# Kernel tuning notes

Measured on AMD Instinct MI355X. Metric: run time of the kernel, lower is better.

## Reference

```python
import jax, jax.numpy as jnp
import numpy as np

N_NODES = 100000
D_FEAT = 64
HIDDEN = 64
N_CLASSES = 16
N_EDGES = 1600000


def setup_inputs() -> dict:
    key = jax.random.key(0)
    ks = jax.random.split(key, 8)
    x = jax.random.normal(ks[0], (N_NODES, D_FEAT), dtype=jnp.float32)
    edge_index = jax.random.randint(ks[1], (2, N_EDGES), 0, N_NODES, dtype=jnp.int64)
    s1 = 1.0 / np.sqrt(D_FEAT)
    s2 = 1.0 / np.sqrt(HIDDEN)
    W1 = jax.random.uniform(ks[2], (D_FEAT, HIDDEN), jnp.float32, -s1, s1)
    b1 = jnp.zeros((HIDDEN,), jnp.float32)
    W2 = jax.random.uniform(ks[3], (HIDDEN, HIDDEN), jnp.float32, -s2, s2)
    b2 = jnp.zeros((HIDDEN,), jnp.float32)
    Wfc = jax.random.uniform(ks[4], (HIDDEN, N_CLASSES), jnp.float32, -s2, s2)
    bfc = jax.random.uniform(ks[5], (N_CLASSES,), jnp.float32, -s2, s2)
    return {"x": x, "edge_index": edge_index, "W1": W1, "b1": b1,
            "W2": W2, "b2": b2, "Wfc": Wfc, "bfc": bfc}


def reference(x, edge_index, W1, b1, W2, b2, Wfc, bfc):
    N = x.shape[0]
    loops = jnp.arange(N, dtype=edge_index.dtype)
    # GCNConv adds self-loops by default
    src = jnp.concatenate([edge_index[0], loops])  # message source j
    dst = jnp.concatenate([edge_index[1], loops])  # aggregation target i
    # symmetric normalization: D^{-1/2} (A + I) D^{-1/2}, degree counted on targets
    deg = jax.ops.segment_sum(jnp.ones_like(dst, dtype=x.dtype), dst, num_segments=N)
    dinv = jnp.where(deg > 0, jax.lax.rsqrt(deg), 0.0)
    norm = dinv[src] * dinv[dst]  # [E+N]

    def gcn_conv(h, W, b):
        h = h @ W                              # [N, out] dense transform first (PyG order)
        msg = h[src] * norm[:, None]            # gather + edge scaling, [E+N, out]
        return jax.ops.segment_sum(msg, dst, num_segments=N) + b

    h = jax.nn.relu(gcn_conv(x, W1, b1))
    # dropout is identity in eval mode
    h = jax.nn.relu(gcn_conv(h, W2, b2))
    return jax.nn.softmax(h @ Wfc + bfc, axis=1)
```

## Files before the change

### kernel.cpp

```cpp
#include <hip/hip_runtime.h>
#include <hip/hip_fp16.h>
#include <math.h>

#define NNODES 100000
#define BSHIFT 7
#define BSIZE 128
#define NBUCK ((NNODES + BSIZE - 1) >> BSHIFT)
#define SCAT_BLOCKS 512
#define CHUNKCAP 3328
#define CAPSHIFT 12
#define BCAP (1 << CAPSHIFT)

__global__ __launch_bounds__(1024) void k_init(int* __restrict__ bcur) {
    int k = blockIdx.x * 1024 + threadIdx.x;
    if (k < NBUCK) bcur[k] = k << CAPSHIFT;
}

__global__ __launch_bounds__(256) void k_scatter_fused(const int* __restrict__ src, const int* __restrict__ dst,
                                                       int* __restrict__ bcur, int* __restrict__ staging,
                                                       int E, int chunk) {
    __shared__ int epack[CHUNKCAP];
    __shared__ unsigned short ebuck[CHUNKCAP];
    __shared__ int hist[NBUCK];
    __shared__ int lcur[NBUCK];
    int t = threadIdx.x;
    for (int k = t; k < NBUCK; k += 256) hist[k] = 0;
    __syncthreads();
    int c0 = blockIdx.x * chunk;
    int c1 = min(E, c0 + chunk);
    int n = c1 - c0;
    for (int j = t; j < n; j += 256) {
        int d = dst[c0 + j];
        int s = src[c0 + j];
        int b = d >> BSHIFT;
        epack[j] = (s << BSHIFT) | (d & (BSIZE - 1));
        ebuck[j] = (unsigned short)b;
        atomicAdd(&hist[b], 1);
    }
    __syncthreads();
    for (int k = t; k < NBUCK; k += 256) {
        int c = hist[k];
        lcur[k] = c ? atomicAdd(&bcur[k], c) : 0;
    }
    __syncthreads();
    for (int j = t; j < n; j += 256) {
        int pos = atomicAdd(&lcur[ebuck[j]], 1);
        staging[pos] = epack[j];
    }
}

__global__ __launch_bounds__(256) void k_bucket_csr(const int* __restrict__ staging, const int* __restrict__ bcur,
                                                    int* __restrict__ rowptr, int* __restrict__ rowend,
                                                    int* __restrict__ ssort, float* __restrict__ dinv, int N) {
    __shared__ int lcnt[BSIZE], lpre[BSIZE];
    int b = blockIdx.x, t = threadIdx.x;
    int node0 = b << BSHIFT;
    int bbase = b << CAPSHIFT;
    int bend = bcur[b];
    if (t < BSIZE) lcnt[t] = 0;
    __syncthreads();
    for (int e = bbase + t; e < bend; e += 256)
        atomicAdd(&lcnt[staging[e] & (BSIZE - 1)], 1);
    __syncthreads();
    if (t < BSIZE) lpre[t] = lcnt[t];
    __syncthreads();
    #pragma unroll
    for (int off = 1; off < BSIZE; off <<= 1) {
        int u = 0;
        if (t < BSIZE && t >= off) u = lpre[t - off];
        __syncthreads();
        if (t < BSIZE) lpre[t] += u;
        __syncthreads();
    }
    if (t < BSIZE) {
        int node = node0 + t;
        if (node < N) {
            int beg = bbase + lpre[t] - lcnt[t];
            rowptr[node] = beg;
            rowend[node] = beg + lcnt[t];
            dinv[node] = rsqrtf((float)(lcnt[t] + 1));
        }
        lpre[t] -= lcnt[t];
    }
    __syncthreads();
    for (int e = bbase + t; e < bend; e += 256) {
        int p = staging[e];
        int pos = atomicAdd(&lpre[p & (BSIZE - 1)], 1);
        ssort[bbase + pos] = p >> BSHIFT;
    }
}

__global__ __launch_bounds__(128) void k_transform2(const float* __restrict__ X, const float* __restrict__ W,
                                                    const float* __restrict__ dinv, __half* __restrict__ Gh, int N) {
    __shared__ float Xs[128 * 65];
    __shared__ float Ws[64 * 64];
    int t = threadIdx.x;
    int node0 = blockIdx.x << 7;
    {
        const float4* W4 = (const float4*)W;
        float4* Ws4 = (float4*)Ws;
        #pragma unroll
        for (int j = 0; j < 8; j++) Ws4[j * 128 + t] = W4[j * 128 + t];
    }
    {
        const float4* X4 = (const float4*)X;
        int lim4 = N << 4;
        #pragma unroll
        for (int ii = 0; ii < 16; ii++) {
            int f = ii * 128 + t;
            int row = f >> 4, cq = f & 15;
            int gi = (node0 << 4) + f;
            float4 v = make_float4(0.f, 0.f, 0.f, 0.f);
            if (gi < lim4) v = X4[gi];
            *(float4*)&Xs[row * 65 + cq * 4] = v;
        }
    }
    __syncthreads();
    float acc[64];
    #pragma unroll
    for (int c = 0; c < 64; c++) acc[c] = 0.f;
    int xbase = t * 65;
    for (int k = 0; k < 64; k++) {
        float xk = Xs[xbase + k];
        const float4* wr = (const float4*)&Ws[k * 64];
        #pragma unroll
        for (int cb = 0; cb < 16; cb++) {
            float4 w4 = wr[cb];
            acc[cb * 4 + 0] = fmaf(xk, w4.x, acc[cb * 4 + 0]);
            acc[cb * 4 + 1] = fmaf(xk, w4.y, acc[cb * 4 + 1]);
            acc[cb * 4 + 2] = fmaf(xk, w4.z, acc[cb * 4 + 2]);
            acc[cb * 4 + 3] = fmaf(xk, w4.w, acc[cb * 4 + 3]);
        }
    }
    int node = node0 + t;
    if (node < N) {
        float di = dinv[node];
        float4* g4 = (float4*)(Gh + (size_t)node * 64);
        #pragma unroll
        for (int cb = 0; cb < 8; cb++) {
            float4 pack;
            __half2* hp = (__half2*)&pack;
            #pragma unroll
            for (int q = 0; q < 4; q++)
                hp[q] = __floats2half2_rn(acc[cb * 8 + 2 * q] * di, acc[cb * 8 + 2 * q + 1] * di);
            g4[cb] = pack;
        }
    }
}

__global__ __launch_bounds__(256) void k_agg(const __half* __restrict__ G, const int* __restrict__ rowptr,
                                             const int* __restrict__ rowend, const int* __restrict__ ssort,
                                             const float* __restrict__ dinv, const float* __restrict__ bias,
                                             float* __restrict__ O, int N) {
    int lane = threadIdx.x & 63;
    int wid = threadIdx.x >> 6;
    int sub = lane >> 3;
    int l = lane & 7;
    int i = blockIdx.x * 4 + wid;
    if (i >= N) return;
    int beg = rowptr[i], end = rowend[i];
    float a[8] = {0.f, 0.f, 0.f, 0.f, 0.f, 0.f, 0.f, 0.f};
    int e = beg + sub;
    for (; e + 8 < end; e += 16) {
        int s0 = ssort[e];
        int s1 = ssort[e + 8];
        float4 g0 = *(const float4*)(G + (size_t)s0 * 64 + 8 * l);
        float4 g1 = *(const float4*)(G + (size_t)s1 * 64 + 8 * l);
        const __half2* h0 = (const __half2*)&g0;
        const __half2* h1 = (const __half2*)&g1;
        #pragma unroll
        for (int q = 0; q < 4; q++) {
            float2 f0 = __half22float2(h0[q]);
            float2 f1 = __half22float2(h1[q]);
            a[2 * q]     += f0.x + f1.x;
            a[2 * q + 1] += f0.y + f1.y;
        }
    }
    if (e < end) {
        int s0 = ssort[e];
        float4 g0 = *(const float4*)(G + (size_t)s0 * 64 + 8 * l);
        const __half2* h0 = (const __half2*)&g0;
        #pragma unroll
        for (int q = 0; q < 4; q++) {
            float2 f0 = __half22float2(h0[q]);
            a[2 * q]     += f0.x;
            a[2 * q + 1] += f0.y;
        }
    }
    #pragma unroll
    for (int mask = 8; mask <= 32; mask <<= 1) {
        #pragma unroll
        for (int q = 0; q < 8; q++) a[q] += __shfl_xor(a[q], mask);
    }
    if (sub == 0) {
        float4 gs = *(const float4*)(G + (size_t)i * 64 + 8 * l);
        const __half2* hs = (const __half2*)&gs;
        #pragma unroll
        for (int q = 0; q < 4; q++) {
            float2 fs = __half22float2(hs[q]);
            a[2 * q]     += fs.x;
            a[2 * q + 1] += fs.y;
        }
        float di = dinv[i];
        float4 b0 = *(const float4*)(bias + 8 * l);
        float4 b1 = *(const float4*)(bias + 8 * l + 4);
        float4 o0, o1;
        o0.x = fmaxf(fmaf(di, a[0], b0.x), 0.f);
        o0.y = fmaxf(fmaf(di, a[1], b0.y), 0.f);
        o0.z = fmaxf(fmaf(di, a[2], b0.z), 0.f);
        o0.w = fmaxf(fmaf(di, a[3], b0.w), 0.f);
        o1.x = fmaxf(fmaf(di, a[4], b1.x), 0.f);
        o1.y = fmaxf(fmaf(di, a[5], b1.y), 0.f);
        o1.z = fmaxf(fmaf(di, a[6], b1.z), 0.f);
        o1.w = fmaxf(fmaf(di, a[7], b1.w), 0.f);
        *(float4*)(O + (size_t)i * 64 + 8 * l) = o0;
        *(float4*)(O + (size_t)i * 64 + 8 * l + 4) = o1;
    }
}

__global__ __launch_bounds__(256) void k_fc_softmax(const float* __restrict__ H, const float* __restrict__ Wfc,
                                                    const float* __restrict__ bfc, float* __restrict__ O, int N) {
    __shared__ float wf[64 * 16];
    __shared__ float bf[16];
    int t = threadIdx.x;
    for (int k = t; k < 1024; k += 256) wf[k] = Wfc[k];
    if (t < 16) bf[t] = bfc[t];
    __syncthreads();
    int gid = blockIdx.x * 256 + t;
    int node = gid >> 4;
    int c = gid & 15;
    if (node >= N) return;
    const float4* hv = (const float4*)(H + (size_t)node * 64);
    float acc = bf[c];
    #pragma unroll
    for (int kk = 0; kk < 16; kk++) {
        float4 h4 = hv[kk];
        acc = fmaf(h4.x, wf[(4 * kk + 0) * 16 + c], acc);
        acc = fmaf(h4.y, wf[(4 * kk + 1) * 16 + c], acc);
        acc = fmaf(h4.z, wf[(4 * kk + 2) * 16 + c], acc);
        acc = fmaf(h4.w, wf[(4 * kk + 3) * 16 + c], acc);
    }
    float m = acc;
    #pragma unroll
    for (int mask = 1; mask < 16; mask <<= 1) m = fmaxf(m, __shfl_xor(m, mask));
    float ex = expf(acc - m);
    float s = ex;
    #pragma unroll
    for (int mask = 1; mask < 16; mask <<= 1) s += __shfl_xor(s, mask);
    O[(size_t)node * 16 + c] = ex / s;
}

extern "C" void kernel_launch(void* const* d_in, const int* in_sizes, int n_in,
                              void* d_out, int out_size, void* d_ws, size_t ws_size,
                              hipStream_t stream) {
    const float* x   = (const float*)d_in[0];
    const int*   ei  = (const int*)d_in[1];
    const float* W1  = (const float*)d_in[2];
    const float* b1  = (const float*)d_in[3];
    const float* W2  = (const float*)d_in[4];
    const float* b2  = (const float*)d_in[5];
    const float* Wfc = (const float*)d_in[6];
    const float* bfc = (const float*)d_in[7];
    float* out = (float*)d_out;
    const int N = NNODES;
    const int E = in_sizes[1] / 2;

    char* ws = (char*)d_ws;
    size_t off = 0;
    auto take = [&](size_t bytes) {
        char* p = ws + off;
        off = (off + bytes + 255) & ~(size_t)255;
        return p;
    };
    int*    staging = (int*)take((size_t)NBUCK * BCAP * 4);
    int*    ssort   = (int*)take((size_t)NBUCK * BCAP * 4);
    float*  bufB    = (float*)take((size_t)N * 64 * 4);
    __half* Gh      = (__half*)take((size_t)N * 64 * 2);
    int*    rowptr  = (int*)take((size_t)N * 4);
    int*    rowend  = (int*)take((size_t)N * 4);
    float*  dinv    = (float*)take((size_t)N * 4);
    int*    bcur    = (int*)take((size_t)NBUCK * 4);

    const int* e_src = ei;
    const int* e_dst = ei + E;

    int chunk = (E + SCAT_BLOCKS - 1) / SCAT_BLOCKS;
    k_init<<<1, 1024, 0, stream>>>(bcur);
    k_scatter_fused<<<SCAT_BLOCKS, 256, 0, stream>>>(e_src, e_dst, bcur, staging, E, chunk);
    k_bucket_csr<<<NBUCK, 256, 0, stream>>>(staging, bcur, rowptr, rowend, ssort, dinv, N);

    int tb = (N + 127) / 128;
    k_transform2<<<tb, 128, 0, stream>>>(x, W1, dinv, Gh, N);
    k_agg<<<(N + 3) / 4, 256, 0, stream>>>(Gh, rowptr, rowend, ssort, dinv, b1, bufB, N);
    k_transform2<<<tb, 128, 0, stream>>>(bufB, W2, dinv, Gh, N);
    k_agg<<<(N + 3) / 4, 256, 0, stream>>>(Gh, rowptr, rowend, ssort, dinv, b2, bufB, N);
    k_fc_softmax<<<(N * 16 + 255) / 256, 256, 0, stream>>>(bufB, Wfc, bfc, out, N);
}
```

Baseline: 224.5 us.

## Restructure dense transform: per-lane output column with weights in registers

The node-feature transform kernel is rewritten so each lane owns one output column and keeps its 64-entry weight column in registers, while a wavefront walks 32 nodes four at a time, reading X rows from LDS as broadcasts. This replaces the old scheme of one node per thread with 64 accumulators and the W tile held in LDS. Blocks grow to 256 threads, and dinv is staged in shared memory. Output is now written as one half per lane, coalesced across the wavefront, instead of 16-byte packed rows per thread. This may cost store efficiency.

```diff
diff --git a/kernel.cpp b/kernel.cpp
--- a/kernel.cpp
+++ b/kernel.cpp
@@ -90,60 +90,67 @@
     }
 }
 
-__global__ __launch_bounds__(128) void k_transform2(const float* __restrict__ X, const float* __restrict__ W,
+__global__ __launch_bounds__(256) void k_transform3(const float* __restrict__ X, const float* __restrict__ W,
                                                     const float* __restrict__ dinv, __half* __restrict__ Gh, int N) {
-    __shared__ float Xs[128 * 65];
-    __shared__ float Ws[64 * 64];
+    __shared__ float4 Xs[2048];
+    __shared__ float dinvs[128];
     int t = threadIdx.x;
+    int lane = t & 63;
     int node0 = blockIdx.x << 7;
-    {
-        const float4* W4 = (const float4*)W;
-        float4* Ws4 = (float4*)Ws;
-        #pragma unroll
-        for (int j = 0; j < 8; j++) Ws4[j * 128 + t] = W4[j * 128 + t];
-    }
     {
         const float4* X4 = (const float4*)X;
         int lim4 = N << 4;
-        #pragma unroll
-        for (int ii = 0; ii < 16; ii++) {
-            int f = ii * 128 + t;
-            int row = f >> 4, cq = f & 15;
-            int gi = (node0 << 4) + f;
-            float4 v = make_float4(0.f, 0.f, 0.f, 0.f);
-            if (gi < lim4) v = X4[gi];
-            *(float4*)&Xs[row * 65 + cq * 4] = v;
-        }
-    }
-    __syncthreads();
-    float acc[64];
-    #pragma unroll
-    for (int c = 0; c < 64; c++) acc[c] = 0.f;
-    int xbase = t * 65;
-    for (int k = 0; k < 64; k++) {
-        float xk = Xs[xbase + k];
-        const float4* wr = (const float4*)&Ws[k * 64];
-        #pragma unroll
-        for (int cb = 0; cb < 16; cb++) {
-            float4 w4 = wr[cb];
-            acc[cb * 4 + 0] = fmaf(xk, w4.x, acc[cb * 4 + 0]);
-            acc[cb * 4 + 1] = fmaf(xk, w4.y, acc[cb * 4 + 1]);
-            acc[cb * 4 + 2] = fmaf(xk, w4.z, acc[cb * 4 + 2]);
-            acc[cb * 4 + 3] = fmaf(xk, w4.w, acc[cb * 4 + 3]);
-        }
-    }
-    int node = node0 + t;
-    if (node < N) {
-        float di = dinv[node];
-        float4* g4 = (float4*)(Gh + (size_t)node * 64);
-        #pragma unroll
-        for (int cb = 0; cb < 8; cb++) {
-            float4 pack;
-            __half2* hp = (__half2*)&pack;
-            #pragma unroll
-            for (int q = 0; q < 4; q++)
-                hp[q] = __floats2half2_rn(acc[cb * 8 + 2 * q] * di, acc[cb * 8 + 2 * q + 1] * di);
-            g4[cb] = pack;
+        int gbase = node0 << 4;
+        #pragma unroll
+        for (int j = 0; j < 8; j++) {
+            int f = j * 256 + t;
+            int gi = gbase + f;
+            Xs[f] = (gi < lim4) ? X4[gi] : make_float4(0.f, 0.f, 0.f, 0.f);
+        }
+    }
+    if (t < 128) {
+        int nd = node0 + t;
+        dinvs[t] = (nd < N) ? dinv[nd] : 0.f;
+    }
+    float w[64];
+    #pragma unroll
+    for (int k = 0; k < 64; k++) w[k] = W[k * 64 + lane];
+    __syncthreads();
+    int woff = (t >> 6) * 32;
+    for (int nn = 0; nn < 32; nn += 4) {
+        const float4* r0 = &Xs[(woff + nn + 0) * 16];
+        const float4* r1 = &Xs[(woff + nn + 1) * 16];
+        const float4* r2 = &Xs[(woff + nn + 2) * 16];
+        const float4* r3 = &Xs[(woff + nn + 3) * 16];
+        float a0 = 0.f, a1 = 0.f, a2 = 0.f, a3 = 0.f;
+        #pragma unroll
+        for (int kq = 0; kq < 16; kq++) {
+            float4 xa = r0[kq];
+            float4 xb = r1[kq];
+            float4 xc = r2[kq];
+            float4 xd = r3[kq];
+            a0 = fmaf(xa.x, w[4*kq+0], a0); a0 = fmaf(xa.y, w[4*kq+1], a0);
+            a0 = fmaf(xa.z, w[4*kq+2], a0); a0 = fmaf(xa.w, w[4*kq+3], a0);
+            a1 = fmaf(xb.x, w[4*kq+0], a1); a1 = fmaf(xb.y, w[4*kq+1], a1);
+            a1 = fmaf(xb.z, w[4*kq+2], a1); a1 = fmaf(xb.w, w[4*kq+3], a1);
+            a2 = fmaf(xc.x, w[4*kq+0], a2); a2 = fmaf(xc.y, w[4*kq+1], a2);
+            a2 = fmaf(xc.z, w[4*kq+2], a2); a2 = fmaf(xc.w, w[4*kq+3], a2);
+            a3 = fmaf(xd.x, w[4*kq+0], a3); a3 = fmaf(xd.y, w[4*kq+1], a3);
+            a3 = fmaf(xd.z, w[4*kq+2], a3); a3 = fmaf(xd.w, w[4*kq+3], a3);
+        }
+        int nb = node0 + woff + nn;
+        float d0 = dinvs[woff+nn+0], d1 = dinvs[woff+nn+1];
+        float d2 = dinvs[woff+nn+2], d3 = dinvs[woff+nn+3];
+        if (nb + 3 < N) {
+            Gh[(size_t)(nb+0)*64 + lane] = __float2half(a0 * d0);
+            Gh[(size_t)(nb+1)*64 + lane] = __float2half(a1 * d1);
+            Gh[(size_t)(nb+2)*64 + lane] = __float2half(a2 * d2);
+            Gh[(size_t)(nb+3)*64 + lane] = __float2half(a3 * d3);
+        } else {
+            if (nb+0 < N) Gh[(size_t)(nb+0)*64 + lane] = __float2half(a0 * d0);
+            if (nb+1 < N) Gh[(size_t)(nb+1)*64 + lane] = __float2half(a1 * d1);
+            if (nb+2 < N) Gh[(size_t)(nb+2)*64 + lane] = __float2half(a2 * d2);
+            if (nb+3 < N) Gh[(size_t)(nb+3)*64 + lane] = __float2half(a3 * d3);
         }
     }
 }
@@ -290,9 +297,9 @@
     k_bucket_csr<<<NBUCK, 256, 0, stream>>>(staging, bcur, rowptr, rowend, ssort, dinv, N);
 
     int tb = (N + 127) / 128;
-    k_transform2<<<tb, 128, 0, stream>>>(x, W1, dinv, Gh, N);
+    k_transform3<<<tb, 256, 0, stream>>>(x, W1, dinv, Gh, N);
     k_agg<<<(N + 3) / 4, 256, 0, stream>>>(Gh, rowptr, rowend, ssort, dinv, b1, bufB, N);
-    k_transform2<<<tb, 128, 0, stream>>>(bufB, W2, dinv, Gh, N);
+    k_transform3<<<tb, 256, 0, stream>>>(bufB, W2, dinv, Gh, N);
     k_agg<<<(N + 3) / 4, 256, 0, stream>>>(Gh, rowptr, rowend, ssort, dinv, b2, bufB, N);
     k_fc_softmax<<<(N * 16 + 255) / 256, 256, 0, stream>>>(bufB, Wfc, bfc, out, N);
 }
```

After: 210.5 us. -6.2%, faster.
